# Performance work log

Hardware: AMD Instinct MI355X
Metric: run time of the kernel (lower is better)

## Reference

```python
import jax, jax.numpy as jnp
import numpy as np

D_MODEL = 1024
D_FF = 4 * D_MODEL
NUM_EXPERTS = 8
TOP_K = 2
BATCH, SEQ = 2, 2048


def setup_inputs() -> dict:
    key = jax.random.key(0)
    ks = jax.random.split(key, 6)
    s_in = 1.0 / np.sqrt(D_MODEL)
    s_ff = 1.0 / np.sqrt(D_FF)
    x = jax.random.normal(ks[0], (BATCH, SEQ, D_MODEL), dtype=jnp.float32)
    Wg = jax.random.uniform(ks[1], (D_MODEL, NUM_EXPERTS), minval=-s_in, maxval=s_in, dtype=jnp.float32)
    W1 = jax.random.uniform(ks[2], (NUM_EXPERTS, D_MODEL, D_FF), minval=-s_in, maxval=s_in, dtype=jnp.float32)
    b1 = jax.random.uniform(ks[3], (NUM_EXPERTS, D_FF), minval=-s_in, maxval=s_in, dtype=jnp.float32)
    W2 = jax.random.uniform(ks[4], (NUM_EXPERTS, D_FF, D_MODEL), minval=-s_ff, maxval=s_ff, dtype=jnp.float32)
    b2 = jax.random.uniform(ks[5], (NUM_EXPERTS, D_MODEL), minval=-s_ff, maxval=s_ff, dtype=jnp.float32)
    return {"x": x, "Wg": Wg, "W1": W1, "b1": b1, "W2": W2, "b2": b2}


def reference(x, Wg, W1, b1, W2, b2):
    B, S, D = x.shape
    x_flat = x.reshape(-1, D)                      # [T, D]
    gate_logits = x_flat @ Wg                      # [T, E] (eval mode: no noise)
    gate_probs = jax.nn.softmax(gate_logits, axis=-1)
    top_v, top_i = jax.lax.top_k(gate_probs, TOP_K)            # [T, k]
    top_v = top_v / (jnp.sum(top_v, axis=-1, keepdims=True) + 1e-8)
    out = jnp.zeros_like(x_flat)
    for e in range(NUM_EXPERTS):
        # combine weight for expert e: sum of normalized top-k probs routed here
        w_e = jnp.sum(jnp.where(top_i == e, top_v, 0.0), axis=-1)   # [T]
        h = jax.nn.gelu(x_flat @ W1[e] + b1[e], approximate=False)  # [T, F]
        y = h @ W2[e] + b2[e]                                       # [T, D]
        out = out + w_e[:, None] * y
    return out.reshape(B, S, D)
```

## Files before the change

kernel.cpp:

```cpp
#include <hip/hip_runtime.h>
#include <math.h>

typedef __attribute__((ext_vector_type(8))) short short8;
typedef __attribute__((ext_vector_type(4))) float f32x4;
typedef unsigned short u16;

#define NT 4096
#define DM 1024
#define DF 4096
#define NE 8
#define HROWS 9216
#define TIT 72
#define YROWS (2 * NT + 8)

static __device__ __forceinline__ u16 f2bf(float f) {
  union { float f; unsigned u; } v; v.f = f;
  return (u16)((v.u + 0x7fffu + ((v.u >> 16) & 1u)) >> 16);
}

static __device__ __forceinline__ float fast_gelu(float x) {
  float x2 = x * x;
  float z = x * __builtin_fmaf(x2, 0.1029392294f, 2.302118131f);
  float e, r;
  asm("v_exp_f32 %0, %1" : "=v"(e) : "v"(z));
  float e1 = e + 1.0f;
  asm("v_rcp_f32 %0, %1" : "=v"(r) : "v"(e1));
  return __builtin_fmaf(-x, r, x);
}

static __device__ __forceinline__ void gload16(const void* g, void* l) {
  __builtin_amdgcn_global_load_lds((const __attribute__((address_space(1))) void*)g,
                                   (__attribute__((address_space(3))) void*)l, 16, 0, 0);
}

static __device__ __forceinline__ int xcd_swz(int bid, int nwg) {
  int per = nwg >> 3;
  return (bid & 7) * per + (bid >> 3);
}

__global__ __launch_bounds__(256) void gate_k(const float* __restrict__ x,
                                              const float* __restrict__ Wg,
                                              int* __restrict__ te,
                                              float* __restrict__ tw,
                                              u16* __restrict__ xbf) {
  int t = blockIdx.x * 4 + (threadIdx.x >> 6);
  int l = threadIdx.x & 63;
  float a0=0,a1=0,a2=0,a3=0,a4=0,a5=0,a6=0,a7=0;
  const float* xr = x + (size_t)t * DM;
  for (int k = l; k < DM; k += 64) {
    float xv = xr[k];
    const float4* wp = (const float4*)(Wg + k * 8);
    float4 w0 = wp[0], w1 = wp[1];
    a0 += xv * w0.x; a1 += xv * w0.y; a2 += xv * w0.z; a3 += xv * w0.w;
    a4 += xv * w1.x; a5 += xv * w1.y; a6 += xv * w1.z; a7 += xv * w1.w;
  }
  u16* xo = xbf + (size_t)t * DM;
#pragma unroll
  for (int h = 0; h < 2; ++h) {
    int k = h * 512 + l * 8;
    float4 a = *(const float4*)(xr + k);
    float4 b = *(const float4*)(xr + k + 4);
    short8 o8 = { (short)f2bf(a.x), (short)f2bf(a.y), (short)f2bf(a.z), (short)f2bf(a.w),
                  (short)f2bf(b.x), (short)f2bf(b.y), (short)f2bf(b.z), (short)f2bf(b.w) };
    *(short8*)(xo + k) = o8;
  }
#pragma unroll
  for (int s = 32; s >= 1; s >>= 1) {
    a0 += __shfl_down(a0, s); a1 += __shfl_down(a1, s);
    a2 += __shfl_down(a2, s); a3 += __shfl_down(a3, s);
    a4 += __shfl_down(a4, s); a5 += __shfl_down(a5, s);
    a6 += __shfl_down(a6, s); a7 += __shfl_down(a7, s);
  }
  if (l == 0) {
    float lg[8] = {a0,a1,a2,a3,a4,a5,a6,a7};
    float m = lg[0];
#pragma unroll
    for (int e = 1; e < 8; ++e) m = fmaxf(m, lg[e]);
    float p[8], s = 0.f;
#pragma unroll
    for (int e = 0; e < 8; ++e) { p[e] = expf(lg[e] - m); s += p[e]; }
#pragma unroll
    for (int e = 0; e < 8; ++e) p[e] /= s;
    int i0 = 0; float v0 = p[0];
#pragma unroll
    for (int e = 1; e < 8; ++e) if (p[e] > v0) { v0 = p[e]; i0 = e; }
    int i1 = -1; float v1 = -1.f;
#pragma unroll
    for (int e = 0; e < 8; ++e) {
      if (e == i0) continue;
      if (p[e] > v1) { v1 = p[e]; i1 = e; }
    }
    float norm = v0 + v1 + 1e-8f;
    te[t*2]   = i0; te[t*2+1] = i1;
    tw[t*2]   = v0 / norm; tw[t*2+1] = v1 / norm;
  }
}

__global__ __launch_bounds__(256) void route_k(const int* __restrict__ te,
                                               const float* __restrict__ tw,
                                               int* __restrict__ meta,
                                               int* __restrict__ lt,
                                               float* __restrict__ lw) {
  int i = blockIdx.x * 256 + threadIdx.x;
  if (i >= NT * 2) return;
  int e = te[i];
  float w = tw[i];
  int pos = atomicAdd(&meta[e], 1);
  lt[e * NT + pos] = i;
  lw[e * NT + pos] = w;
}

__global__ __launch_bounds__(256) void finalize_k(int* __restrict__ meta,
                                                  int* __restrict__ lt,
                                                  float* __restrict__ lw) {
  __shared__ int s_cnt[8], s_pc[8];
  if (threadIdx.x == 0) {
    int base = 0, nt_ = 0;
    for (int e = 0; e < 8; ++e) {
      int c = meta[e];
      int pc = (c + 127) & ~127;
      s_cnt[e] = c; s_pc[e] = pc;
      meta[8 + e] = pc;
      meta[16 + e] = base;
      base += pc;
      for (int mt = 0; mt < pc / 128; ++mt) meta[32 + nt_++] = (e << 16) | mt;
    }
    meta[24] = nt_;
  }
  __syncthreads();
  for (int e = 0; e < 8; ++e) {
    int c = s_cnt[e], pc = s_pc[e];
    for (int i = c + (int)threadIdx.x; i < pc; i += 256) {
      lt[e * NT + i] = 2 * NT;
      lw[e * NT + i] = 0.f;
    }
  }
}

static __device__ __forceinline__ void prep_tile(const float* __restrict__ ie,
                                                 u16* __restrict__ oe,
                                                 int K, int N, int k0, int n0) {
  __shared__ u16 t[64 * 72];
  const int tid = threadIdx.x;
  const int kr = tid >> 4, nq = (tid & 15) * 4;
#pragma unroll
  for (int it = 0; it < 4; ++it) {
    int k = it * 16 + kr;
    float4 v = *(const float4*)(ie + (size_t)(k0 + k) * N + n0 + nq);
    t[(nq + 0) * 72 + k] = f2bf(v.x);
    t[(nq + 1) * 72 + k] = f2bf(v.y);
    t[(nq + 2) * 72 + k] = f2bf(v.z);
    t[(nq + 3) * 72 + k] = f2bf(v.w);
  }
  __syncthreads();
#pragma unroll
  for (int it = 0; it < 2; ++it) {
    int idx = it * 256 + tid;
    int n = idx >> 3, kc = idx & 7;
    short8 v = *(const short8*)&t[n * 72 + kc * 8];
    *(short8*)(oe + (size_t)(n0 + n) * K + k0 + kc * 8) = v;
  }
}

__global__ __launch_bounds__(256) void prep_wT(const float* __restrict__ in,
                                               u16* __restrict__ out, int K, int N) {
  const int e = blockIdx.z;
  prep_tile(in + (size_t)e * K * N, out + (size_t)e * K * N,
            K, N, blockIdx.y * 64, blockIdx.x * 64);
}

__global__ __launch_bounds__(256) void prep_both(const float* __restrict__ W1,
                                                 const float* __restrict__ W2,
                                                 u16* __restrict__ W1T,
                                                 u16* __restrict__ W2T) {
  int bid = blockIdx.x;
  if (bid < 8192) {
    int e = bid >> 10, rem = bid & 1023;
    prep_tile(W1 + (size_t)e * DM * DF, W1T + (size_t)e * DM * DF,
              DM, DF, (rem >> 6) * 64, (rem & 63) * 64);
  } else {
    bid -= 8192;
    int e = bid >> 10, rem = bid & 1023;
    prep_tile(W2 + (size_t)e * DF * DM, W2T + (size_t)e * DF * DM,
              DF, DM, (rem >> 4) * 64, (rem & 15) * 64);
  }
}

__global__ __launch_bounds__(256) void ffn1_k(const u16* __restrict__ xbf,
                                              const u16* __restrict__ W1T,
                                              const float* __restrict__ b1,
                                              const int* __restrict__ lt,
                                              const int* __restrict__ meta,
                                              u16* __restrict__ H) {
  const int vid = xcd_swz(blockIdx.x, (DF / 128) * TIT);
  const int nt = vid & 31;
  const int ti = vid >> 5;
  if (ti >= meta[24]) return;
  const int em = meta[32 + ti];
  const int e = em >> 16, mt = em & 0xffff;
  const int rbase = meta[16 + e];

  __shared__ u16 As[128 * 32];
  __shared__ u16 Bs[128 * 32];

  const int tid = threadIdx.x, lane = tid & 63, wv = tid >> 6;
  const int wm = wv >> 1, wn = wv & 1, l15 = lane & 15, l4 = lane >> 4;

  int r0i = tid >> 2, s0 = tid & 3;
  int r1i = (256 + tid) >> 2;
  int kg0 = s0 ^ ((r0i >> 1) & 3);
  int kg1 = s0 ^ ((r1i >> 1) & 3);
  int tok0 = lt[e * NT + mt * 128 + r0i] >> 1; if (tok0 >= NT) tok0 = 0;
  int tok1 = lt[e * NT + mt * 128 + r1i] >> 1; if (tok1 >= NT) tok1 = 0;
  const u16* pa0 = xbf + (size_t)tok0 * DM + kg0 * 8;
  const u16* pa1 = xbf + (size_t)tok1 * DM + kg1 * 8;
  const u16* pb0 = W1T + ((size_t)e * DF + nt * 128 + r0i) * DM + kg0 * 8;
  const u16* pb1 = W1T + ((size_t)e * DF + nt * 128 + r1i) * DM + kg1 * 8;
  const int lda0 = (wv * 64) * 8, lda1 = (256 + wv * 64) * 8;

  int aoff[4], boff[4];
#pragma unroll
  for (int i = 0; i < 4; ++i) {
    int ra = wm * 64 + i * 16 + l15;
    aoff[i] = ra * 32 + (l4 ^ ((ra >> 1) & 3)) * 8;
    int rb = wn * 64 + i * 16 + l15;
    boff[i] = rb * 32 + (l4 ^ ((rb >> 1) & 3)) * 8;
  }

  f32x4 acc[4][4];
#pragma unroll
  for (int mi = 0; mi < 4; ++mi)
#pragma unroll
    for (int ni = 0; ni < 4; ++ni) acc[mi][ni] = 0.f;

  const int NK = DM / 32;
  for (int ks = 0; ks < NK; ++ks) {
    __syncthreads();
    gload16(pa0, As + lda0); gload16(pa1, As + lda1);
    gload16(pb0, Bs + lda0); gload16(pb1, Bs + lda1);
    pa0 += 32; pa1 += 32; pb0 += 32; pb1 += 32;
    __syncthreads();

    short8 af[4], bf_[4];
#pragma unroll
    for (int i = 0; i < 4; ++i) {
      af[i]  = *(const short8*)&As[aoff[i]];
      bf_[i] = *(const short8*)&Bs[boff[i]];
    }
#pragma unroll
    for (int mi = 0; mi < 4; ++mi)
#pragma unroll
      for (int ni = 0; ni < 4; ++ni)
        acc[mi][ni] = __builtin_amdgcn_mfma_f32_16x16x32_bf16(af[mi], bf_[ni], acc[mi][ni], 0, 0, 0);
  }

  const size_t hrow0 = (size_t)rbase + mt * 128;
#pragma unroll
  for (int mi = 0; mi < 4; ++mi) {
#pragma unroll
    for (int ni = 0; ni < 4; ++ni) {
      int gn = nt * 128 + wn * 64 + ni * 16 + l15;
      float bias = b1[e * DF + gn];
      int rr = wm * 64 + mi * 16 + l4 * 4;
#pragma unroll
      for (int j = 0; j < 4; ++j) {
        float v = fast_gelu(acc[mi][ni][j] + bias);
        H[(hrow0 + rr + j) * DF + gn] = f2bf(v);
      }
    }
  }
}

template <bool USEY>
__global__ __launch_bounds__(256) void ffn2_k(const u16* __restrict__ H,
                                              const u16* __restrict__ W2T,
                                              const float* __restrict__ b2,
                                              const int* __restrict__ lt,
                                              const float* __restrict__ lw,
                                              const int* __restrict__ meta,
                                              float* __restrict__ Y,
                                              float* __restrict__ out) {
  const int vid = xcd_swz(blockIdx.x, (DM / 128) * TIT);
  const int nt = vid & 7;
  const int ti = vid >> 3;
  if (ti >= meta[24]) return;
  const int em = meta[32 + ti];
  const int e = em >> 16, mt = em & 0xffff;
  const int rbase = meta[16 + e];

  __shared__ u16 As[128 * 32];
  __shared__ u16 Bs[128 * 32];
  __shared__ int s_ts[128];
  __shared__ float s_w[128];

  const int tid = threadIdx.x, lane = tid & 63, wv = tid >> 6;
  const int wm = wv >> 1, wn = wv & 1, l15 = lane & 15, l4 = lane >> 4;

  if (tid < 128) {
    s_ts[tid] = lt[e * NT + mt * 128 + tid];
    s_w[tid]  = lw[e * NT + mt * 128 + tid];
  }

  int r0i = tid >> 2, s0 = tid & 3;
  int r1i = (256 + tid) >> 2;
  int kg0 = s0 ^ ((r0i >> 1) & 3);
  int kg1 = s0 ^ ((r1i >> 1) & 3);
  const u16* pa0 = H + ((size_t)rbase + mt * 128 + r0i) * DF + kg0 * 8;
  const u16* pa1 = H + ((size_t)rbase + mt * 128 + r1i) * DF + kg1 * 8;
  const u16* pb0 = W2T + ((size_t)e * DM + nt * 128 + r0i) * DF + kg0 * 8;
  const u16* pb1 = W2T + ((size_t)e * DM + nt * 128 + r1i) * DF + kg1 * 8;
  const int lda0 = (wv * 64) * 8, lda1 = (256 + wv * 64) * 8;

  int aoff[4], boff[4];
#pragma unroll
  for (int i = 0; i < 4; ++i) {
    int ra = wm * 64 + i * 16 + l15;
    aoff[i] = ra * 32 + (l4 ^ ((ra >> 1) & 3)) * 8;
    int rb = wn * 64 + i * 16 + l15;
    boff[i] = rb * 32 + (l4 ^ ((rb >> 1) & 3)) * 8;
  }

  f32x4 acc[4][4];
#pragma unroll
  for (int mi = 0; mi < 4; ++mi)
#pragma unroll
    for (int ni = 0; ni < 4; ++ni) acc[mi][ni] = 0.f;

  const int NK = DF / 32;
  for (int ks = 0; ks < NK; ++ks) {
    __syncthreads();
    gload16(pa0, As + lda0); gload16(pa1, As + lda1);
    gload16(pb0, Bs + lda0); gload16(pb1, Bs + lda1);
    pa0 += 32; pa1 += 32; pb0 += 32; pb1 += 32;
    __syncthreads();

    short8 af[4], bf_[4];
#pragma unroll
    for (int i = 0; i < 4; ++i) {
      af[i]  = *(const short8*)&As[aoff[i]];
      bf_[i] = *(const short8*)&Bs[boff[i]];
    }
#pragma unroll
    for (int mi = 0; mi < 4; ++mi)
#pragma unroll
      for (int ni = 0; ni < 4; ++ni)
        acc[mi][ni] = __builtin_amdgcn_mfma_f32_16x16x32_bf16(af[mi], bf_[ni], acc[mi][ni], 0, 0, 0);
  }

#pragma unroll
  for (int mi = 0; mi < 4; ++mi) {
#pragma unroll
    for (int ni = 0; ni < 4; ++ni) {
      int gn = nt * 128 + wn * 64 + ni * 16 + l15;
      float bias = b2[e * DM + gn];
      int rr = wm * 64 + mi * 16 + l4 * 4;
#pragma unroll
      for (int j = 0; j < 4; ++j) {
        int r = rr + j;
        float w = s_w[r];
        int ts = s_ts[r];
        float v = w * (acc[mi][ni][j] + bias);
        if (USEY) {
          Y[(size_t)ts * DM + gn] = v;
        } else {
          int tok = ts >> 1;
          if (tok >= NT) tok = 0;
          atomicAdd(out + (size_t)tok * DM + gn, v);
        }
      }
    }
  }
}

__global__ __launch_bounds__(256) void combine_k(const float* __restrict__ Y,
                                                 float* __restrict__ out) {
  size_t i4 = (size_t)blockIdx.x * 256 + threadIdx.x;
  size_t t = i4 >> 8;
  int c4 = (int)(i4 & 255) * 4;
  const float4 a = *(const float4*)(Y + (2 * t) * DM + c4);
  const float4 b = *(const float4*)(Y + (2 * t + 1) * DM + c4);
  float4 o = { a.x + b.x, a.y + b.y, a.z + b.z, a.w + b.w };
  *(float4*)(out + t * DM + c4) = o;
}

extern "C" void kernel_launch(void* const* d_in, const int* in_sizes, int n_in,
                              void* d_out, int out_size, void* d_ws, size_t ws_size,
                              hipStream_t stream) {
  const float* x  = (const float*)d_in[0];
  const float* Wg = (const float*)d_in[1];
  const float* W1 = (const float*)d_in[2];
  const float* b1 = (const float*)d_in[3];
  const float* W2 = (const float*)d_in[4];
  const float* b2 = (const float*)d_in[5];
  float* out = (float*)d_out;

  char* ws = (char*)d_ws;
  size_t o = 0;
  auto take = [&](size_t sz) { size_t p = o; o = (o + sz + 1023) & ~(size_t)1023; return p; };

  int*   meta = (int*)(ws + take(1024));
  int*   te   = (int*)(ws + take((size_t)NT * 2 * 4));
  float* tw   = (float*)(ws + take((size_t)NT * 2 * 4));
  int*   lt   = (int*)(ws + take((size_t)NE * NT * 4));
  float* lw   = (float*)(ws + take((size_t)NE * NT * 4));
  u16*   xbf  = (u16*)(ws + take((size_t)NT * DM * 2));
  u16*   W1T  = (u16*)(ws + take((size_t)NE * DM * DF * 2));
  u16*   H    = (u16*)(ws + take((size_t)HROWS * DF * 2));
  size_t needB = o;
  size_t ySz = (size_t)YROWS * DM * 4;
  size_t needA = needB + ((size_t)NE * DM * DF * 2 + 1024) + (ySz + 1024);

  bool pathA = (ws_size >= needA);
  u16*   W2T;
  float* Y = nullptr;
  if (pathA) {
    W2T = (u16*)(ws + take((size_t)NE * DM * DF * 2));
    Y   = (float*)(ws + take(ySz));
  } else {
    W2T = W1T;
  }

  hipMemsetAsync(meta, 0, 1024, stream);
  if (!pathA) hipMemsetAsync(out, 0, (size_t)NT * DM * 4, stream);

  gate_k<<<NT / 4, 256, 0, stream>>>(x, Wg, te, tw, xbf);
  route_k<<<(NT * 2) / 256, 256, 0, stream>>>(te, tw, meta, lt, lw);
  finalize_k<<<1, 256, 0, stream>>>(meta, lt, lw);

  if (pathA) {
    prep_both<<<16384, 256, 0, stream>>>(W1, W2, W1T, W2T);
  } else {
    prep_wT<<<dim3(DF / 64, DM / 64, NE), 256, 0, stream>>>(W1, W1T, DM, DF);
  }

  ffn1_k<<<(DF / 128) * TIT, 256, 0, stream>>>(xbf, W1T, b1, lt, meta, H);

  if (!pathA)
    prep_wT<<<dim3(DM / 64, DF / 64, NE), 256, 0, stream>>>(W2, W2T, DF, DM);

  if (pathA) {
    ffn2_k<true><<<(DM / 128) * TIT, 256, 0, stream>>>(H, W2T, b2, lt, lw, meta, Y, out);
    combine_k<<<NT, 256, 0, stream>>>(Y, out);
  } else {
    ffn2_k<false><<<(DM / 128) * TIT, 256, 0, stream>>>(H, W2T, b2, lt, lw, meta, Y, out);
  }
}
```

Before: 352.4 us.

## Load MFMA operands directly from global memory, removing LDS staging and barriers

Both expert GEMM kernels stop staging A/B tiles through shared memory with two barriers per K step. Each lane now loads its MFMA fragments straight from global memory via per-row pointers, and the K loop is unrolled by 8. This removes LDS traffic and synchronisation, but gives up data sharing between waves: every operand is fetched redundantly by two waves, and each lane reads a small 16-byte piece per row, so the kernels depend on L1/L2 to absorb the extra traffic.

```diff
diff --git a/kernel.cpp b/kernel.cpp
--- a/kernel.cpp
+++ b/kernel.cpp
@@ -26,11 +26,6 @@
   float e1 = e + 1.0f;
   asm("v_rcp_f32 %0, %1" : "=v"(r) : "v"(e1));
   return __builtin_fmaf(-x, r, x);
-}
-
-static __device__ __forceinline__ void gload16(const void* g, void* l) {
-  __builtin_amdgcn_global_load_lds((const __attribute__((address_space(1))) void*)g,
-                                   (__attribute__((address_space(3))) void*)l, 16, 0, 0);
 }
 
 static __device__ __forceinline__ int xcd_swz(int bid, int nwg) {
@@ -200,31 +195,17 @@
   const int e = em >> 16, mt = em & 0xffff;
   const int rbase = meta[16 + e];
 
-  __shared__ u16 As[128 * 32];
-  __shared__ u16 Bs[128 * 32];
-
   const int tid = threadIdx.x, lane = tid & 63, wv = tid >> 6;
   const int wm = wv >> 1, wn = wv & 1, l15 = lane & 15, l4 = lane >> 4;
 
-  int r0i = tid >> 2, s0 = tid & 3;
-  int r1i = (256 + tid) >> 2;
-  int kg0 = s0 ^ ((r0i >> 1) & 3);
-  int kg1 = s0 ^ ((r1i >> 1) & 3);
-  int tok0 = lt[e * NT + mt * 128 + r0i] >> 1; if (tok0 >= NT) tok0 = 0;
-  int tok1 = lt[e * NT + mt * 128 + r1i] >> 1; if (tok1 >= NT) tok1 = 0;
-  const u16* pa0 = xbf + (size_t)tok0 * DM + kg0 * 8;
-  const u16* pa1 = xbf + (size_t)tok1 * DM + kg1 * 8;
-  const u16* pb0 = W1T + ((size_t)e * DF + nt * 128 + r0i) * DM + kg0 * 8;
-  const u16* pb1 = W1T + ((size_t)e * DF + nt * 128 + r1i) * DM + kg1 * 8;
-  const int lda0 = (wv * 64) * 8, lda1 = (256 + wv * 64) * 8;
-
-  int aoff[4], boff[4];
+  const u16* pa[4]; const u16* pb[4];
 #pragma unroll
   for (int i = 0; i < 4; ++i) {
     int ra = wm * 64 + i * 16 + l15;
-    aoff[i] = ra * 32 + (l4 ^ ((ra >> 1) & 3)) * 8;
+    int tok = lt[e * NT + mt * 128 + ra] >> 1; if (tok >= NT) tok = 0;
+    pa[i] = xbf + (size_t)tok * DM + l4 * 8;
     int rb = wn * 64 + i * 16 + l15;
-    boff[i] = rb * 32 + (l4 ^ ((rb >> 1) & 3)) * 8;
+    pb[i] = W1T + ((size_t)e * DF + nt * 128 + rb) * DM + l4 * 8;
   }
 
   f32x4 acc[4][4];
@@ -234,24 +215,21 @@
     for (int ni = 0; ni < 4; ++ni) acc[mi][ni] = 0.f;
 
   const int NK = DM / 32;
+#pragma unroll 8
   for (int ks = 0; ks < NK; ++ks) {
-    __syncthreads();
-    gload16(pa0, As + lda0); gload16(pa1, As + lda1);
-    gload16(pb0, Bs + lda0); gload16(pb1, Bs + lda1);
-    pa0 += 32; pa1 += 32; pb0 += 32; pb1 += 32;
-    __syncthreads();
-
     short8 af[4], bf_[4];
 #pragma unroll
     for (int i = 0; i < 4; ++i) {
-      af[i]  = *(const short8*)&As[aoff[i]];
-      bf_[i] = *(const short8*)&Bs[boff[i]];
+      af[i]  = *(const short8*)pa[i];
+      bf_[i] = *(const short8*)pb[i];
     }
 #pragma unroll
     for (int mi = 0; mi < 4; ++mi)
 #pragma unroll
       for (int ni = 0; ni < 4; ++ni)
         acc[mi][ni] = __builtin_amdgcn_mfma_f32_16x16x32_bf16(af[mi], bf_[ni], acc[mi][ni], 0, 0, 0);
+#pragma unroll
+    for (int i = 0; i < 4; ++i) { pa[i] += 32; pb[i] += 32; }
   }
 
   const size_t hrow0 = (size_t)rbase + mt * 128;
@@ -288,36 +266,16 @@
   const int e = em >> 16, mt = em & 0xffff;
   const int rbase = meta[16 + e];
 
-  __shared__ u16 As[128 * 32];
-  __shared__ u16 Bs[128 * 32];
-  __shared__ int s_ts[128];
-  __shared__ float s_w[128];
-
   const int tid = threadIdx.x, lane = tid & 63, wv = tid >> 6;
   const int wm = wv >> 1, wn = wv & 1, l15 = lane & 15, l4 = lane >> 4;
 
-  if (tid < 128) {
-    s_ts[tid] = lt[e * NT + mt * 128 + tid];
-    s_w[tid]  = lw[e * NT + mt * 128 + tid];
-  }
-
-  int r0i = tid >> 2, s0 = tid & 3;
-  int r1i = (256 + tid) >> 2;
-  int kg0 = s0 ^ ((r0i >> 1) & 3);
-  int kg1 = s0 ^ ((r1i >> 1) & 3);
-  const u16* pa0 = H + ((size_t)rbase + mt * 128 + r0i) * DF + kg0 * 8;
-  const u16* pa1 = H + ((size_t)rbase + mt * 128 + r1i) * DF + kg1 * 8;
-  const u16* pb0 = W2T + ((size_t)e * DM + nt * 128 + r0i) * DF + kg0 * 8;
-  const u16* pb1 = W2T + ((size_t)e * DM + nt * 128 + r1i) * DF + kg1 * 8;
-  const int lda0 = (wv * 64) * 8, lda1 = (256 + wv * 64) * 8;
-
-  int aoff[4], boff[4];
+  const u16* pa[4]; const u16* pb[4];
 #pragma unroll
   for (int i = 0; i < 4; ++i) {
     int ra = wm * 64 + i * 16 + l15;
-    aoff[i] = ra * 32 + (l4 ^ ((ra >> 1) & 3)) * 8;
+    pa[i] = H + ((size_t)rbase + mt * 128 + ra) * DF + l4 * 8;
     int rb = wn * 64 + i * 16 + l15;
-    boff[i] = rb * 32 + (l4 ^ ((rb >> 1) & 3)) * 8;
+    pb[i] = W2T + ((size_t)e * DM + nt * 128 + rb) * DF + l4 * 8;
   }
 
   f32x4 acc[4][4];
@@ -327,39 +285,36 @@
     for (int ni = 0; ni < 4; ++ni) acc[mi][ni] = 0.f;
 
   const int NK = DF / 32;
+#pragma unroll 8
   for (int ks = 0; ks < NK; ++ks) {
-    __syncthreads();
-    gload16(pa0, As + lda0); gload16(pa1, As + lda1);
-    gload16(pb0, Bs + lda0); gload16(pb1, Bs + lda1);
-    pa0 += 32; pa1 += 32; pb0 += 32; pb1 += 32;
-    __syncthreads();
-
     short8 af[4], bf_[4];
 #pragma unroll
     for (int i = 0; i < 4; ++i) {
-      af[i]  = *(const short8*)&As[aoff[i]];
-      bf_[i] = *(const short8*)&Bs[boff[i]];
+      af[i]  = *(const short8*)pa[i];
+      bf_[i] = *(const short8*)pb[i];
     }
 #pragma unroll
     for (int mi = 0; mi < 4; ++mi)
 #pragma unroll
       for (int ni = 0; ni < 4; ++ni)
         acc[mi][ni] = __builtin_amdgcn_mfma_f32_16x16x32_bf16(af[mi], bf_[ni], acc[mi][ni], 0, 0, 0);
-  }
-
+#pragma unroll
+    for (int i = 0; i < 4; ++i) { pa[i] += 32; pb[i] += 32; }
+  }
+
+  const int lbase = e * NT + mt * 128;
 #pragma unroll
   for (int mi = 0; mi < 4; ++mi) {
-#pragma unroll
-    for (int ni = 0; ni < 4; ++ni) {
-      int gn = nt * 128 + wn * 64 + ni * 16 + l15;
-      float bias = b2[e * DM + gn];
-      int rr = wm * 64 + mi * 16 + l4 * 4;
-#pragma unroll
-      for (int j = 0; j < 4; ++j) {
-        int r = rr + j;
-        float w = s_w[r];
-        int ts = s_ts[r];
-        float v = w * (acc[mi][ni][j] + bias);
+    int rr = wm * 64 + mi * 16 + l4 * 4;
+#pragma unroll
+    for (int j = 0; j < 4; ++j) {
+      int r = rr + j;
+      int ts = lt[lbase + r];
+      float w = lw[lbase + r];
+#pragma unroll
+      for (int ni = 0; ni < 4; ++ni) {
+        int gn = nt * 128 + wn * 64 + ni * 16 + l15;
+        float v = w * (acc[mi][ni][j] + b2[e * DM + gn]);
         if (USEY) {
           Y[(size_t)ts * DM + gn] = v;
         } else {
```

Result: slower. 769.4 us (+118.4%).
